# Optimization experiments

Hardware: AMD Instinct MI355X
Metric: run time of the kernel (lower is better)

The kernel has to match this reference:

```python
import jax, jax.numpy as jnp
import numpy as np

DIM = 2048
NH = 16
HD = DIM // NH          # 128
ROPE = 64               # qk_rope_head_dim
B = 2
S = 2048
LAYER_ID = 12
LAMBDA_INIT = float(0.8 - 0.6 * np.exp(-0.3 * LAYER_ID))
EPS = 1e-5


def _rope(x, cos, sin):
    # interleaved RoPE: pairs (x[2i], x[2i+1]) rotated by angle; x: [b,s,h,ROPE]
    xr = x[..., 0::2]
    xi = x[..., 1::2]
    c = cos[None, :, None, :]  # [1,s,1,ROPE/2]
    s_ = sin[None, :, None, :]
    yr = xr * c - xi * s_
    yi = xr * s_ + xi * c
    return jnp.stack([yr, yi], axis=-1).reshape(x.shape)


def _rope_head(t, cos, sin):
    # apply RoPE to first ROPE dims of head_dim, pass-through the rest
    return jnp.concatenate([_rope(t[..., :ROPE], cos, sin), t[..., ROPE:]], axis=-1)


def setup_inputs() -> dict:
    key = jax.random.key(0)
    ks = jax.random.split(key, 10)
    inner = 2 * NH * HD
    x = jax.random.normal(ks[0], (B, S, DIM), jnp.float32)
    w_q = jax.random.normal(ks[1], (inner, DIM), jnp.float32) * (DIM ** -0.5)
    w_k = jax.random.normal(ks[2], (inner, DIM), jnp.float32) * (DIM ** -0.5)
    w_v = jax.random.normal(ks[3], (inner, DIM), jnp.float32) * (DIM ** -0.5)
    w_o = jax.random.normal(ks[4], (DIM, inner), jnp.float32) * (inner ** -0.5)
    # lambda reparameterization params (paper uses small-std init for stability)
    lambda_q1 = jax.random.normal(ks[5], (NH, HD), jnp.float32) * 0.1
    lambda_k1 = jax.random.normal(ks[6], (NH, HD), jnp.float32) * 0.1
    lambda_q2 = jax.random.normal(ks[7], (NH, HD), jnp.float32) * 0.1
    lambda_k2 = jax.random.normal(ks[8], (NH, HD), jnp.float32) * 0.1
    rms_scale = jnp.ones((NH, 2 * HD), jnp.float32)
    # rotary frequencies
    pos = jnp.arange(S, dtype=jnp.float32)
    inv_freq = 1.0 / (10000.0 ** (jnp.arange(0, ROPE, 2, dtype=jnp.float32) / ROPE))
    ang = pos[:, None] * inv_freq[None, :]  # [S, ROPE/2]
    freqs_cos = jnp.cos(ang)
    freqs_sin = jnp.sin(ang)
    # additive causal mask
    mask = jnp.triu(jnp.full((S, S), -1e9, jnp.float32), k=1)
    return dict(x=x, w_q=w_q, w_k=w_k, w_v=w_v, w_o=w_o,
                lambda_q1=lambda_q1, lambda_k1=lambda_k1,
                lambda_q2=lambda_q2, lambda_k2=lambda_k2,
                rms_scale=rms_scale, freqs_cos=freqs_cos, freqs_sin=freqs_sin,
                mask=mask)


def reference(x, w_q, w_k, w_v, w_o, lambda_q1, lambda_k1, lambda_q2, lambda_k2,
              rms_scale, freqs_cos, freqs_sin, mask):
    b, s, _ = x.shape
    q = (x @ w_q.T).reshape(b, s, NH, 2 * HD)
    k = (x @ w_k.T).reshape(b, s, NH, 2 * HD)
    v = (x @ w_v.T).reshape(b, s, NH, 2 * HD)
    q1, q2 = jnp.split(q, 2, axis=-1)
    k1, k2 = jnp.split(k, 2, axis=-1)
    q1 = _rope_head(q1, freqs_cos, freqs_sin)
    q2 = _rope_head(q2, freqs_cos, freqs_sin)
    k1 = _rope_head(k1, freqs_cos, freqs_sin)
    k2 = _rope_head(k2, freqs_cos, freqs_sin)
    # start_pos = 0 prefill -> cache slice equals current k/v
    scale = HD ** -0.5
    s1 = jnp.einsum('bqhd,bkhd->bhqk', q1, k1) * scale + mask[None, None]
    s2 = jnp.einsum('bqhd,bkhd->bhqk', q2, k2) * scale + mask[None, None]
    a1 = jax.nn.softmax(s1, axis=-1)
    a2 = jax.nn.softmax(s2, axis=-1)
    lam1 = jnp.exp(jnp.sum(lambda_q1 * lambda_k1, axis=-1))  # [NH]
    lam2 = jnp.exp(jnp.sum(lambda_q2 * lambda_k2, axis=-1))
    lam = lam1 - lam2 + LAMBDA_INIT
    attn = a1 - lam[None, :, None, None] * a2
    o = jnp.einsum('bhqk,bkhd->bqhd', attn, v)  # [b,s,NH,2*HD]
    # headwise RMSNorm over 2*head_dim, then (1 - lambda_init) scaling
    o = o * jax.lax.rsqrt(jnp.mean(o * o, axis=-1, keepdims=True) + EPS)
    o = o * rms_scale[None, None] * (1.0 - LAMBDA_INIT)
    return o.reshape(b, s, 2 * NH * HD) @ w_o.T
```

## Files before the change

kernel.cpp:

```cpp
#include <hip/hip_runtime.h>

typedef __attribute__((ext_vector_type(8))) short s16x8;
typedef __attribute__((ext_vector_type(4))) short s16x4;
typedef __attribute__((ext_vector_type(4))) float f32x4;

#define NHh   16
#define Sd    2048
#define Bb    2
#define MSd   4096
#define DIMd  2048
#define INNERd 4096

constexpr float LAMBDA_INIT = 0.7836057665f;
constexpr float POST_SCALE  = 1.0f - LAMBDA_INIT;
constexpr float QK_SCALE    = 0.08838834764831845f;
constexpr float EPSf        = 1e-5f;

__device__ __forceinline__ short f2bf(float x) {
  unsigned u = __builtin_bit_cast(unsigned, x);
  u = (u + 0x7fffu + ((u >> 16) & 1u)) >> 16;
  return (short)u;
}
__device__ __forceinline__ float bf2f(short x) {
  unsigned u = ((unsigned)(unsigned short)x) << 16;
  return __builtin_bit_cast(float, u);
}
__device__ __forceinline__ f32x4 mfma16(s16x8 a, s16x8 b, f32x4 c) {
  return __builtin_amdgcn_mfma_f32_16x16x32_bf16(a, b, c, 0, 0, 0);
}
__device__ __forceinline__ void async16(void* lds, const void* g) {
  __builtin_amdgcn_global_load_lds(
      (const __attribute__((address_space(1))) void*)g,
      (__attribute__((address_space(3))) void*)lds, 16, 0, 0);
}

__global__ __launch_bounds__(256)
void convert5(const float* __restrict__ a0, const float* __restrict__ a1,
              const float* __restrict__ a2, const float* __restrict__ a3,
              const float* __restrict__ a4,
              short* __restrict__ o0, short* __restrict__ o1,
              short* __restrict__ o2, short* __restrict__ o3,
              short* __restrict__ o4) {
  const float* src; short* dst;
  switch (blockIdx.y) {
    case 0: src = a0; dst = o0; break;
    case 1: src = a1; dst = o1; break;
    case 2: src = a2; dst = o2; break;
    case 3: src = a3; dst = o3; break;
    default: src = a4; dst = o4; break;
  }
  size_t i = ((size_t)blockIdx.x * 256 + threadIdx.x) * 4;
  f32x4 x = *(const f32x4*)(src + i);
  s16x4 o;
#pragma unroll
  for (int j = 0; j < 4; ++j) o[j] = f2bf(x[j]);
  *(s16x4*)(dst + i) = o;
}

__global__ void lambda_kernel(const float* __restrict__ lq1, const float* __restrict__ lk1,
                              const float* __restrict__ lq2, const float* __restrict__ lk2,
                              float* __restrict__ lam) {
  int h = threadIdx.x;
  if (h < NHh) {
    float s1 = 0.f, s2 = 0.f;
    for (int d = 0; d < 128; ++d) {
      s1 += lq1[h * 128 + d] * lk1[h * 128 + d];
      s2 += lq2[h * 128 + d] * lk2[h * 128 + d];
    }
    lam[h] = expf(s1) - expf(s2) + LAMBDA_INIT;
  }
}

template <typename OutT>
__global__ __launch_bounds__(256)
void gemm_bt(const short* __restrict__ A, const short* __restrict__ Bm,
             OutT* __restrict__ C, int M, int N, int K) {
  __shared__ __align__(16) short As[128 * 32];
  __shared__ __align__(16) short Bs[128 * 32];
  const int tid  = threadIdx.x;
  const int lane = tid & 63;
  const int w    = tid >> 6;
  const int wr   = (w >> 1) * 64;
  const int wc   = (w & 1) * 64;

  const int nb  = gridDim.x * gridDim.y;
  const int id  = blockIdx.y * gridDim.x + blockIdx.x;
  const int cpx = nb >> 3;
  const int sw  = (id & 7) * cpx + (id >> 3);
  const int m0  = (sw % gridDim.x) * 128;
  const int n0  = (sw / gridDim.x) * 128;

  const int l15  = lane & 15, l4 = lane >> 4;

  f32x4 acc[4][4] = {};

  for (int kt = 0; kt < K; kt += 32) {
#pragma unroll
    for (int j = 0; j < 2; ++j) {
      int L  = j * 4096 + tid * 16;
      int r  = L >> 6;
      int s  = (L >> 4) & 3;
      int sp = s ^ ((r >> 1) & 3);
      async16((char*)As + L, A  + (size_t)(m0 + r) * K + kt + sp * 8);
      async16((char*)Bs + L, Bm + (size_t)(n0 + r) * K + kt + sp * 8);
    }
    __syncthreads();

    s16x8 af[4], bf[4];
#pragma unroll
    for (int mi = 0; mi < 4; ++mi) {
      int r  = wr + mi * 16 + l15;
      int sl = l4 ^ ((r >> 1) & 3);
      af[mi] = *(const s16x8*)(As + r * 32 + sl * 8);
    }
#pragma unroll
    for (int ni = 0; ni < 4; ++ni) {
      int r  = wc + ni * 16 + l15;
      int sl = l4 ^ ((r >> 1) & 3);
      bf[ni] = *(const s16x8*)(Bs + r * 32 + sl * 8);
    }
#pragma unroll
    for (int mi = 0; mi < 4; ++mi)
#pragma unroll
      for (int ni = 0; ni < 4; ++ni)
        acc[mi][ni] = mfma16(af[mi], bf[ni], acc[mi][ni]);
    __syncthreads();
  }

#pragma unroll
  for (int mi = 0; mi < 4; ++mi)
#pragma unroll
    for (int ni = 0; ni < 4; ++ni)
#pragma unroll
      for (int j = 0; j < 4; ++j) {
        int row = m0 + wr + mi * 16 + l4 * 4 + j;
        int col = n0 + wc + ni * 16 + l15;
        float v = acc[mi][ni][j];
        if constexpr (sizeof(OutT) == 2) C[(size_t)row * N + col] = f2bf(v);
        else                             C[(size_t)row * N + col] = v;
      }
}

__global__ __launch_bounds__(256)
void rope_qk(short* __restrict__ qp, short* __restrict__ kp,
             const float* __restrict__ fc, const float* __restrict__ fs) {
  int idx  = blockIdx.x * 256 + threadIdx.x;
  int ib   = idx & 7;
  int half = (idx >> 3) & 1;
  int h    = (idx >> 4) & 15;
  int s    = (idx >> 8) & 2047;
  int b    = (idx >> 19) & 1;
  short* base = (idx >> 20) ? kp : qp;
  size_t off  = ((size_t)(b * Sd + s) * NHh + h) * 256 + half * 128 + ib * 8;
  s16x8 v = *(s16x8*)(base + off);
  f32x4 c  = *(const f32x4*)(fc + s * 32 + ib * 4);
  f32x4 sn = *(const f32x4*)(fs + s * 32 + ib * 4);
#pragma unroll
  for (int p = 0; p < 4; ++p) {
    float xr = bf2f(v[2 * p]), xi = bf2f(v[2 * p + 1]);
    float yr = xr * c[p] - xi * sn[p];
    float yi = xr * sn[p] + xi * c[p];
    v[2 * p]     = f2bf(yr);
    v[2 * p + 1] = f2bf(yi);
  }
  *(s16x8*)(base + off) = v;
}

__global__ __launch_bounds__(256)
void transpose_v(const short* __restrict__ v, short* __restrict__ vt) {
  __shared__ __align__(16) short t[64][80];
  const int s0 = blockIdx.x * 64;
  const int d0 = blockIdx.y * 64;
  const int bh = blockIdx.z;
  const int b  = bh >> 4, h = bh & 15;
  const int tid = threadIdx.x;
#pragma unroll
  for (int rp = 0; rp < 2; ++rp) {
    int i  = rp * 256 + tid;
    int sl = i >> 3;
    int dl = (i & 7) * 8;
    s16x8 x = *(const s16x8*)(v + ((size_t)(b * Sd + s0 + sl) * NHh + h) * 256 + d0 + dl);
    *(s16x8*)(&t[sl][dl]) = x;
  }
  __syncthreads();
#pragma unroll
  for (int rp = 0; rp < 2; ++rp) {
    int i   = rp * 256 + tid;
    int dl  = i >> 3;
    int sp8 = (i & 7) * 8;
    s16x8 x;
#pragma unroll
    for (int j = 0; j < 8; ++j) x[j] = t[sp8 + j][dl];
    *(s16x8*)(vt + ((size_t)bh * 256 + d0 + dl) * Sd + s0 + sp8) = x;
  }
}

__global__ __launch_bounds__(256)
void flash_one(const short* __restrict__ q, const short* __restrict__ k,
               const short* __restrict__ vt,
               short* __restrict__ o1b, short* __restrict__ o2b) {
  const int qt  = gridDim.x - 1 - blockIdx.x;
  const int h   = blockIdx.y >> 1;
  const int mat = blockIdx.y & 1;
  const int b   = blockIdx.z;
  const int tid = threadIdx.x;
  const int lane = tid & 63, w = tid >> 6;
  const int q0 = qt * 64;
  const int wrow0 = q0 + w * 16;
  const int l15 = lane & 15, l4 = lane >> 4;

  __shared__ __align__(16) short Ks[32 * 128];
  __shared__ __align__(16) short Vs[256 * 32];
  __shared__ __align__(16) short Ps[4][16 * 40];

  s16x8 qf[4];
  {
    const size_t qrow = ((size_t)(b * Sd + wrow0 + l15) * NHh + h) * 256 + mat * 128;
#pragma unroll
    for (int kb = 0; kb < 4; ++kb)
      qf[kb] = *(const s16x8*)(q + qrow + kb * 32 + l4 * 8);
  }

  float m[4], l[4];
#pragma unroll
  for (int j = 0; j < 4; ++j) { m[j] = -1e30f; l[j] = 0.f; }
  f32x4 O[16] = {};

  const int kv_end = q0 + 64;
  for (int kv0 = 0; kv0 < kv_end; kv0 += 32) {
#pragma unroll
    for (int j = 0; j < 2; ++j) {
      int L  = j * 4096 + tid * 16;
      int r  = L >> 8;
      int s  = (L >> 4) & 15;
      int sp = s ^ (r & 7);
      async16((char*)Ks + L,
              k + ((size_t)(b * Sd + kv0 + r) * NHh + h) * 256 + mat * 128 + sp * 8);
    }
#pragma unroll
    for (int j = 0; j < 4; ++j) {
      int L  = j * 4096 + tid * 16;
      int r  = L >> 6;
      int s  = (L >> 4) & 3;
      int sp = s ^ ((r >> 1) & 3);
      async16((char*)Vs + L, vt + ((size_t)(b * NHh + h) * 256 + r) * Sd + kv0 + sp * 8);
    }
    __syncthreads();

    if (kv0 <= wrow0 + 15) {
      f32x4 s[2] = {};
#pragma unroll
      for (int kb = 0; kb < 4; ++kb)
#pragma unroll
        for (int cf = 0; cf < 2; ++cf) {
          int r  = cf * 16 + l15;
          int sl = (kb * 4 + l4) ^ (r & 7);
          s16x8 kf = *(const s16x8*)(Ks + r * 128 + sl * 8);
          s[cf] = mfma16(qf[kb], kf, s[cf]);
        }

      float sv[2][4];
#pragma unroll
      for (int cf = 0; cf < 2; ++cf)
#pragma unroll
        for (int j = 0; j < 4; ++j) {
          int kvc = kv0 + cf * 16 + l15;
          int row = wrow0 + l4 * 4 + j;
          sv[cf][j] = (kvc > row) ? -1e9f : s[cf][j] * QK_SCALE;
        }

      float tmax[4], rs[4], ps[4];
#pragma unroll
      for (int j = 0; j < 4; ++j) tmax[j] = fmaxf(sv[0][j], sv[1][j]);
#pragma unroll
      for (int j = 0; j < 4; ++j) {
        tmax[j] = fmaxf(tmax[j], __shfl_xor(tmax[j], 1));
        tmax[j] = fmaxf(tmax[j], __shfl_xor(tmax[j], 2));
        tmax[j] = fmaxf(tmax[j], __shfl_xor(tmax[j], 4));
        tmax[j] = fmaxf(tmax[j], __shfl_xor(tmax[j], 8));
      }
#pragma unroll
      for (int j = 0; j < 4; ++j) {
        float mn = fmaxf(m[j], tmax[j]);
        rs[j] = __expf(m[j] - mn);
        m[j] = mn;
        ps[j] = 0.f;
      }
#pragma unroll
      for (int cf = 0; cf < 2; ++cf)
#pragma unroll
        for (int j = 0; j < 4; ++j) {
          float p = __expf(sv[cf][j] - m[j]);
          ps[j] += p;
          Ps[w][(l4 * 4 + j) * 40 + cf * 16 + l15] = f2bf(p);
        }
#pragma unroll
      for (int j = 0; j < 4; ++j) {
        ps[j] += __shfl_xor(ps[j], 1);
        ps[j] += __shfl_xor(ps[j], 2);
        ps[j] += __shfl_xor(ps[j], 4);
        ps[j] += __shfl_xor(ps[j], 8);
        l[j] = l[j] * rs[j] + ps[j];
      }
#pragma unroll
      for (int nf = 0; nf < 16; ++nf) {
        O[nf][0] *= rs[0]; O[nf][1] *= rs[1];
        O[nf][2] *= rs[2]; O[nf][3] *= rs[3];
      }

      s16x8 pa = *(const s16x8*)(&Ps[w][0] + l15 * 40 + l4 * 8);
#pragma unroll
      for (int nf = 0; nf < 16; ++nf) {
        int d  = nf * 16 + l15;
        int sl = l4 ^ ((d >> 1) & 3);
        s16x8 vf = *(const s16x8*)(Vs + d * 32 + sl * 8);
        O[nf] = mfma16(pa, vf, O[nf]);
      }
    }
    __syncthreads();
  }

  float inv[4];
#pragma unroll
  for (int j = 0; j < 4; ++j) inv[j] = 1.f / l[j];
  short* dst = mat ? o2b : o1b;
#pragma unroll
  for (int nf = 0; nf < 16; ++nf)
#pragma unroll
    for (int j = 0; j < 4; ++j)
      dst[((size_t)(b * Sd + wrow0 + l4 * 4 + j) * NHh + h) * 256 + nf * 16 + l15] =
          f2bf(O[nf][j] * inv[j]);
}

__global__ __launch_bounds__(256)
void combine(const short* __restrict__ o1b, const short* __restrict__ o2b,
             const float* __restrict__ lam, const float* __restrict__ rms,
             short* __restrict__ ob) {
  const int t = threadIdx.x;
  const int row = blockIdx.x * 16 + (t >> 4);
  const int h = row & 15;
  const int d0 = (t & 15) * 16;
  const size_t base = (size_t)row * 256 + d0;
  const float lamh = lam[h];

  s16x8 a0 = *(const s16x8*)(o1b + base);
  s16x8 a1 = *(const s16x8*)(o1b + base + 8);
  s16x8 b0 = *(const s16x8*)(o2b + base);
  s16x8 b1 = *(const s16x8*)(o2b + base + 8);
  float o[16];
  float ss = 0.f;
#pragma unroll
  for (int j = 0; j < 8; ++j) {
    o[j]     = bf2f(a0[j]) - lamh * bf2f(b0[j]);
    o[8 + j] = bf2f(a1[j]) - lamh * bf2f(b1[j]);
  }
#pragma unroll
  for (int j = 0; j < 16; ++j) ss += o[j] * o[j];
  ss += __shfl_xor(ss, 1);
  ss += __shfl_xor(ss, 2);
  ss += __shfl_xor(ss, 4);
  ss += __shfl_xor(ss, 8);
  const float r = rsqrtf(ss * (1.f / 256.f) + EPSf);

  s16x8 w0, w1;
#pragma unroll
  for (int j = 0; j < 8; ++j) {
    w0[j] = f2bf(o[j]     * r * rms[h * 256 + d0 + j]     * POST_SCALE);
    w1[j] = f2bf(o[8 + j] * r * rms[h * 256 + d0 + 8 + j] * POST_SCALE);
  }
  *(s16x8*)(ob + base)     = w0;
  *(s16x8*)(ob + base + 8) = w1;
}

extern "C" void kernel_launch(void* const* d_in, const int* in_sizes, int n_in,
                              void* d_out, int out_size, void* d_ws, size_t ws_size,
                              hipStream_t stream) {
  const float* x   = (const float*)d_in[0];
  const float* w_q = (const float*)d_in[1];
  const float* w_k = (const float*)d_in[2];
  const float* w_v = (const float*)d_in[3];
  const float* w_o = (const float*)d_in[4];
  const float* lq1 = (const float*)d_in[5];
  const float* lk1 = (const float*)d_in[6];
  const float* lq2 = (const float*)d_in[7];
  const float* lk2 = (const float*)d_in[8];
  const float* rms = (const float*)d_in[9];
  const float* fc  = (const float*)d_in[10];
  const float* fs  = (const float*)d_in[11];

  char* ws = (char*)d_ws;
  const size_t SMb = 16777216ull;
  const size_t BGb = 33554432ull;
  short* xb  = (short*)(ws);
  short* wqb = (short*)(ws + 1 * SMb);
  short* wkb = (short*)(ws + 2 * SMb);
  short* wvb = (short*)(ws + 3 * SMb);
  short* wob = (short*)(ws + 4 * SMb);
  short* qb  = (short*)(ws + 5 * SMb);
  short* kb  = (short*)(ws + 5 * SMb + 1 * BGb);
  short* vb  = (short*)(ws + 5 * SMb + 2 * BGb);
  short* vtb = (short*)(ws + 5 * SMb + 3 * BGb);
  short* ob  = (short*)(ws + 5 * SMb + 4 * BGb);
  float* lam = (float*)(ws + 5 * SMb + 5 * BGb);
  short* o1b = ob;
  short* o2b = (short*)(ws);

  convert5<<<dim3(8192, 5), 256, 0, stream>>>(x, w_q, w_k, w_v, w_o,
                                              xb, wqb, wkb, wvb, wob);
  lambda_kernel<<<1, 64, 0, stream>>>(lq1, lk1, lq2, lk2, lam);
  gemm_bt<short><<<dim3(32, 32), 256, 0, stream>>>(xb, wqb, qb, 4096, 4096, 2048);
  gemm_bt<short><<<dim3(32, 32), 256, 0, stream>>>(xb, wkb, kb, 4096, 4096, 2048);
  gemm_bt<short><<<dim3(32, 32), 256, 0, stream>>>(xb, wvb, vb, 4096, 4096, 2048);
  rope_qk<<<8192, 256, 0, stream>>>(qb, kb, fc, fs);
  transpose_v<<<dim3(32, 4, 32), 256, 0, stream>>>(vb, vtb);
  flash_one<<<dim3(32, 32, 2), 256, 0, stream>>>(qb, kb, vtb, o1b, o2b);
  combine<<<4096, 256, 0, stream>>>(o1b, o2b, lam, rms, ob);
  gemm_bt<float><<<dim3(32, 16), 256, 0, stream>>>(ob, wob, (float*)d_out, 4096, 2048, 4096);
}
```

Baseline: 1.201 ms.

## Load K/V fragments directly from global in flash kernel, remap grid for XCD locality

```diff
diff --git a/kernel.cpp b/kernel.cpp
--- a/kernel.cpp
+++ b/kernel.cpp
@@ -195,23 +195,30 @@
   }
 }
 
-__global__ __launch_bounds__(256)
+__global__ __launch_bounds__(256, 8)
 void flash_one(const short* __restrict__ q, const short* __restrict__ k,
                const short* __restrict__ vt,
                short* __restrict__ o1b, short* __restrict__ o2b) {
-  const int qt  = gridDim.x - 1 - blockIdx.x;
-  const int h   = blockIdx.y >> 1;
-  const int mat = blockIdx.y & 1;
-  const int b   = blockIdx.z;
+  const int d0i = blockIdx.x;
+  const int x  = d0i & 7;
+  const int jj = d0i >> 3;
+  const int lg = jj >> 5;
+  const int c  = jj & 31;
+  const int qt = 31 - ((c + lg * 13) & 31);
+  const int g  = x * 8 + lg;
+  const int h2 = g & 31;
+  const int b  = g >> 5;
+  const int h  = h2 >> 1;
+  const int mat = h2 & 1;
+
   const int tid = threadIdx.x;
   const int lane = tid & 63, w = tid >> 6;
   const int q0 = qt * 64;
   const int wrow0 = q0 + w * 16;
   const int l15 = lane & 15, l4 = lane >> 4;
 
-  __shared__ __align__(16) short Ks[32 * 128];
-  __shared__ __align__(16) short Vs[256 * 32];
-  __shared__ __align__(16) short Ps[4][16 * 40];
+  __shared__ __align__(16) short Ps[4][16 * 72];
+  short* pbuf = &Ps[w][0];
 
   s16x8 qf[4];
   {
@@ -226,98 +233,80 @@
   for (int j = 0; j < 4; ++j) { m[j] = -1e30f; l[j] = 0.f; }
   f32x4 O[16] = {};
 
-  const int kv_end = q0 + 64;
-  for (int kv0 = 0; kv0 < kv_end; kv0 += 32) {
-#pragma unroll
-    for (int j = 0; j < 2; ++j) {
-      int L  = j * 4096 + tid * 16;
-      int r  = L >> 8;
-      int s  = (L >> 4) & 15;
-      int sp = s ^ (r & 7);
-      async16((char*)Ks + L,
-              k + ((size_t)(b * Sd + kv0 + r) * NHh + h) * 256 + mat * 128 + sp * 8);
-    }
+  const short* kb_base = k + ((size_t)b * Sd * NHh) * 256 + (size_t)h * 256 + mat * 128 + l4 * 8;
+  const short* vt_base = vt + ((size_t)(b * NHh + h) * 256 + l15) * Sd + l4 * 8;
+
+  for (int t = 0; t <= qt; ++t) {
+    const int kv0 = t * 64;
+
+    f32x4 s[4] = {};
+#pragma unroll
+    for (int cf = 0; cf < 4; ++cf) {
+      const short* kp = kb_base + (size_t)(kv0 + cf * 16 + l15) * (NHh * 256);
+#pragma unroll
+      for (int kbi = 0; kbi < 4; ++kbi)
+        s[cf] = mfma16(qf[kbi], *(const s16x8*)(kp + kbi * 32), s[cf]);
+    }
+
+    float sv[4][4];
+#pragma unroll
+    for (int cf = 0; cf < 4; ++cf)
+#pragma unroll
+      for (int j = 0; j < 4; ++j) {
+        int kvc = kv0 + cf * 16 + l15;
+        int row = wrow0 + l4 * 4 + j;
+        sv[cf][j] = (kvc > row) ? -1e9f : s[cf][j] * QK_SCALE;
+      }
+
+    float tmax[4], rs[4], ps[4];
+#pragma unroll
+    for (int j = 0; j < 4; ++j)
+      tmax[j] = fmaxf(fmaxf(sv[0][j], sv[1][j]), fmaxf(sv[2][j], sv[3][j]));
 #pragma unroll
     for (int j = 0; j < 4; ++j) {
-      int L  = j * 4096 + tid * 16;
-      int r  = L >> 6;
-      int s  = (L >> 4) & 3;
-      int sp = s ^ ((r >> 1) & 3);
-      async16((char*)Vs + L, vt + ((size_t)(b * NHh + h) * 256 + r) * Sd + kv0 + sp * 8);
-    }
-    __syncthreads();
-
-    if (kv0 <= wrow0 + 15) {
-      f32x4 s[2] = {};
-#pragma unroll
-      for (int kb = 0; kb < 4; ++kb)
-#pragma unroll
-        for (int cf = 0; cf < 2; ++cf) {
-          int r  = cf * 16 + l15;
-          int sl = (kb * 4 + l4) ^ (r & 7);
-          s16x8 kf = *(const s16x8*)(Ks + r * 128 + sl * 8);
-          s[cf] = mfma16(qf[kb], kf, s[cf]);
-        }
-
-      float sv[2][4];
-#pragma unroll
-      for (int cf = 0; cf < 2; ++cf)
-#pragma unroll
-        for (int j = 0; j < 4; ++j) {
-          int kvc = kv0 + cf * 16 + l15;
-          int row = wrow0 + l4 * 4 + j;
-          sv[cf][j] = (kvc > row) ? -1e9f : s[cf][j] * QK_SCALE;
-        }
-
-      float tmax[4], rs[4], ps[4];
-#pragma unroll
-      for (int j = 0; j < 4; ++j) tmax[j] = fmaxf(sv[0][j], sv[1][j]);
+      tmax[j] = fmaxf(tmax[j], __shfl_xor(tmax[j], 1));
+      tmax[j] = fmaxf(tmax[j], __shfl_xor(tmax[j], 2));
+      tmax[j] = fmaxf(tmax[j], __shfl_xor(tmax[j], 4));
+      tmax[j] = fmaxf(tmax[j], __shfl_xor(tmax[j], 8));
+    }
+#pragma unroll
+    for (int j = 0; j < 4; ++j) {
+      float mn = fmaxf(m[j], tmax[j]);
+      rs[j] = __expf(m[j] - mn);
+      m[j] = mn;
+      ps[j] = 0.f;
+    }
+#pragma unroll
+    for (int cf = 0; cf < 4; ++cf)
 #pragma unroll
       for (int j = 0; j < 4; ++j) {
-        tmax[j] = fmaxf(tmax[j], __shfl_xor(tmax[j], 1));
-        tmax[j] = fmaxf(tmax[j], __shfl_xor(tmax[j], 2));
-        tmax[j] = fmaxf(tmax[j], __shfl_xor(tmax[j], 4));
-        tmax[j] = fmaxf(tmax[j], __shfl_xor(tmax[j], 8));
+        float p = __expf(sv[cf][j] - m[j]);
+        ps[j] += p;
+        pbuf[(l4 * 4 + j) * 72 + cf * 16 + l15] = f2bf(p);
       }
 #pragma unroll
-      for (int j = 0; j < 4; ++j) {
-        float mn = fmaxf(m[j], tmax[j]);
-        rs[j] = __expf(m[j] - mn);
-        m[j] = mn;
-        ps[j] = 0.f;
-      }
-#pragma unroll
-      for (int cf = 0; cf < 2; ++cf)
-#pragma unroll
-        for (int j = 0; j < 4; ++j) {
-          float p = __expf(sv[cf][j] - m[j]);
-          ps[j] += p;
-          Ps[w][(l4 * 4 + j) * 40 + cf * 16 + l15] = f2bf(p);
-        }
-#pragma unroll
-      for (int j = 0; j < 4; ++j) {
-        ps[j] += __shfl_xor(ps[j], 1);
-        ps[j] += __shfl_xor(ps[j], 2);
-        ps[j] += __shfl_xor(ps[j], 4);
-        ps[j] += __shfl_xor(ps[j], 8);
-        l[j] = l[j] * rs[j] + ps[j];
-      }
-#pragma unroll
-      for (int nf = 0; nf < 16; ++nf) {
-        O[nf][0] *= rs[0]; O[nf][1] *= rs[1];
-        O[nf][2] *= rs[2]; O[nf][3] *= rs[3];
-      }
-
-      s16x8 pa = *(const s16x8*)(&Ps[w][0] + l15 * 40 + l4 * 8);
-#pragma unroll
-      for (int nf = 0; nf < 16; ++nf) {
-        int d  = nf * 16 + l15;
-        int sl = l4 ^ ((d >> 1) & 3);
-        s16x8 vf = *(const s16x8*)(Vs + d * 32 + sl * 8);
-        O[nf] = mfma16(pa, vf, O[nf]);
-      }
-    }
-    __syncthreads();
+    for (int j = 0; j < 4; ++j) {
+      ps[j] += __shfl_xor(ps[j], 1);
+      ps[j] += __shfl_xor(ps[j], 2);
+      ps[j] += __shfl_xor(ps[j], 4);
+      ps[j] += __shfl_xor(ps[j], 8);
+      l[j] = l[j] * rs[j] + ps[j];
+    }
+#pragma unroll
+    for (int nf = 0; nf < 16; ++nf) {
+      O[nf][0] *= rs[0]; O[nf][1] *= rs[1];
+      O[nf][2] *= rs[2]; O[nf][3] *= rs[3];
+    }
+
+    s16x8 pa0 = *(const s16x8*)(pbuf + l15 * 72 + l4 * 8);
+    s16x8 pa1 = *(const s16x8*)(pbuf + l15 * 72 + 32 + l4 * 8);
+
+#pragma unroll
+    for (int nf = 0; nf < 16; ++nf) {
+      const short* vp = vt_base + (size_t)(nf * 16) * Sd + kv0;
+      O[nf] = mfma16(pa0, *(const s16x8*)vp, O[nf]);
+      O[nf] = mfma16(pa1, *(const s16x8*)(vp + 32), O[nf]);
+    }
   }
 
   float inv[4];
@@ -413,7 +402,7 @@
   gemm_bt<short><<<dim3(32, 32), 256, 0, stream>>>(xb, wvb, vb, 4096, 4096, 2048);
   rope_qk<<<8192, 256, 0, stream>>>(qb, kb, fc, fs);
   transpose_v<<<dim3(32, 4, 32), 256, 0, stream>>>(vb, vtb);
-  flash_one<<<dim3(32, 32, 2), 256, 0, stream>>>(qb, kb, vtb, o1b, o2b);
+  flash_one<<<2048, 256, 0, stream>>>(qb, kb, vtb, o1b, o2b);
   combine<<<4096, 256, 0, stream>>>(o1b, o2b, lam, rms, ob);
   gemm_bt<float><<<dim3(32, 16), 256, 0, stream>>>(ob, wob, (float*)d_out, 4096, 2048, 4096);
 }
```

Measured after the change: 2.416 ms. 2.01x slower.
